# Kernel tuning notes

Measured on AMD Instinct MI355X. Metric: run time of the kernel, lower is better.

## Reference

```python
import jax, jax.numpy as jnp
import numpy as np

E = 16      # num experts
K = 2       # top-k
EPS = np.finfo(float).eps


def setup_inputs() -> dict:
    key = jax.random.key(0)
    k1, k2, k3 = jax.random.split(key, 3)
    B, D_IN, D_OUT = 16384, 1024, 512
    x = jax.random.normal(k1, (B, D_IN), dtype=jnp.float32)
    w_router = jax.random.normal(k2, (D_IN, E), dtype=jnp.float32) * 0.02
    w_experts = jax.random.normal(k3, (E, D_IN, D_OUT), dtype=jnp.float32) * 0.02
    return {"x": x, "w_router": w_router, "w_experts": w_experts}


def reference(x, w_router, w_experts):
    # --- noisy_top_k_gating (eval path: clean logits, no noise) ---
    logits = x @ w_router                      # [B, E]
    top_vals, top_idx = jax.lax.top_k(logits, K)   # [B, K]
    top_gates = jax.nn.softmax(top_vals, axis=1)   # softmax over top-k logits
    B = x.shape[0]
    gates = jnp.zeros_like(logits).at[jnp.arange(B)[:, None], top_idx].set(top_gates)  # [B, E]

    # --- per-expert encode (dense form; zero gates null out non-dispatched pairs,
    #     matching SparseDispatcher's sparse dispatch/combine math exactly) ---
    expert_out = jnp.einsum('bd,edh->beh', x, w_experts)  # [B, E, d_out]

    # --- SparseDispatcher.combine: exp -> gate-weight -> index_add -> eps clamp -> log ---
    combined = jnp.einsum('be,beh->bh', gates, jnp.exp(expert_out))  # [B, d_out]
    combined = jnp.where(combined == 0, jnp.asarray(EPS, combined.dtype), combined)
    return jnp.log(combined)
```

## Files before the change

kernel.cpp:

```cpp
#include <hip/hip_runtime.h>
#include <hip/hip_bf16.h>
#include <stdint.h>

typedef unsigned short u16_t;
typedef unsigned int   u32_t;

#define B_ROWS  16384
#define D_IN    1024
#define D_OUT   512
#define NEXP    16
#define CNT_STRIDE 16
#define EPSF    2.2204460492503131e-16f

using short8  = __attribute__((ext_vector_type(8))) short;
using floatx4 = __attribute__((ext_vector_type(4))) float;

__device__ __forceinline__ u16_t f2bf(float f) {
    u32_t u = __float_as_uint(f);
    u += 0x7fffu + ((u >> 16) & 1u);
    return (u16_t)(u >> 16);
}

__device__ __forceinline__ void gload_lds16(const void* g, void* l) {
    __builtin_amdgcn_global_load_lds(
        (const __attribute__((address_space(1))) void*)g,
        (__attribute__((address_space(3))) void*)l, 16, 0, 0);
}

__global__ __launch_bounds__(256) void prep_kernel(
        const float* __restrict__ wr, float* __restrict__ wrT,
        const float* __restrict__ we, u16_t* __restrict__ wT,
        int* __restrict__ counts) {
    int b = blockIdx.x, t = threadIdx.x;
    if (b < 64) {
        int i = b * 256 + t;
        int e = i >> 10, d = i & 1023;
        wrT[i] = wr[d * NEXP + e];
    } else if (b == 64) {
        counts[t] = 0;
    } else {
        int bb = b - 65;
        int e  = bb >> 8;
        int k0 = ((bb >> 1) & 127) * 8;
        int n  = (bb & 1) * 256 + t;
        const float* src = we + ((size_t)e * D_IN + k0) * D_OUT + n;
        union { u16_t us[8]; uint4 v; } p;
        #pragma unroll
        for (int j = 0; j < 8; ++j) p.us[j] = f2bf(src[(size_t)j * D_OUT]);
        *(uint4*)(wT + ((size_t)e * D_OUT + n) * D_IN + k0) = p.v;
    }
}

__global__ __launch_bounds__(256) void router_kernel(
        const float* __restrict__ x, const float* __restrict__ wrT,
        int* __restrict__ counts, int* __restrict__ rowlist,
        float* __restrict__ gatelist, u16_t* __restrict__ xb) {
    __shared__ int hist[NEXP], base[NEXP], hist2[NEXP];
    __shared__ unsigned char eidx_sh[16][2];
    __shared__ float g_sh[16][2];

    int t = threadIdx.x;
    if (t < NEXP) { hist[t] = 0; hist2[t] = 0; }
    __syncthreads();

    int lr = t >> 5, c = t & 31;
    int row0 = blockIdx.x * 16 + lr * 2;
    const float* xr = x + (size_t)row0 * D_IN + c * 4;
    const float4* wr4 = (const float4*)wrT;

    double acc[2][NEXP];
    #pragma unroll
    for (int rr = 0; rr < 2; ++rr)
        #pragma unroll
        for (int e = 0; e < NEXP; ++e) acc[rr][e] = 0.0;

    for (int i = 0; i < 8; ++i) {
        int d = c * 4 + i * 128;
        float4 xv[2];
        #pragma unroll
        for (int rr = 0; rr < 2; ++rr)
            xv[rr] = *(const float4*)(xr + (size_t)rr * D_IN + i * 128);
        if (xb) {
            #pragma unroll
            for (int rr = 0; rr < 2; ++rr) {
                uint2 pk;
                pk.x = (u32_t)f2bf(xv[rr].x) | ((u32_t)f2bf(xv[rr].y) << 16);
                pk.y = (u32_t)f2bf(xv[rr].z) | ((u32_t)f2bf(xv[rr].w) << 16);
                *(uint2*)(xb + (size_t)(row0 + rr) * D_IN + d) = pk;
            }
        }
        int f4 = c + i * 32;
        #pragma unroll
        for (int e = 0; e < NEXP; ++e) {
            float4 wv = wr4[e * 256 + f4];
            #pragma unroll
            for (int rr = 0; rr < 2; ++rr) {
                acc[rr][e] += (double)xv[rr].x * (double)wv.x;
                acc[rr][e] += (double)xv[rr].y * (double)wv.y;
                acc[rr][e] += (double)xv[rr].z * (double)wv.z;
                acc[rr][e] += (double)xv[rr].w * (double)wv.w;
            }
        }
    }
    #pragma unroll
    for (int rr = 0; rr < 2; ++rr)
        #pragma unroll
        for (int e = 0; e < NEXP; ++e) {
            acc[rr][e] += __shfl_xor(acc[rr][e], 1);
            acc[rr][e] += __shfl_xor(acc[rr][e], 2);
            acc[rr][e] += __shfl_xor(acc[rr][e], 4);
            acc[rr][e] += __shfl_xor(acc[rr][e], 8);
            acc[rr][e] += __shfl_xor(acc[rr][e], 16);
        }
    if (c == 0) {
        #pragma unroll
        for (int rr = 0; rr < 2; ++rr) {
            int i1 = 0; double v1 = acc[rr][0];
            #pragma unroll
            for (int e = 1; e < NEXP; ++e) if (acc[rr][e] > v1) { v1 = acc[rr][e]; i1 = e; }
            int i2 = -1; double v2 = -1.0e300;
            #pragma unroll
            for (int e = 0; e < NEXP; ++e) if (e != i1 && acc[rr][e] > v2) { v2 = acc[rr][e]; i2 = e; }
            double ed = exp(v2 - v1);
            double s = 1.0 + ed;
            int lrow = lr * 2 + rr;
            eidx_sh[lrow][0] = (unsigned char)i1; g_sh[lrow][0] = (float)(1.0 / s);
            eidx_sh[lrow][1] = (unsigned char)i2; g_sh[lrow][1] = (float)(ed / s);
            atomicAdd(&hist[i1], 1);
            atomicAdd(&hist[i2], 1);
        }
    }
    __syncthreads();
    if (t < NEXP) base[t] = atomicAdd(&counts[t * CNT_STRIDE], hist[t]);
    __syncthreads();
    if (t < 32) {
        int r = t >> 1, sl = t & 1;
        int e = eidx_sh[r][sl];
        int pos = base[e] + atomicAdd(&hist2[e], 1);
        rowlist[e * B_ROWS + pos] = ((blockIdx.x * 16 + r) << 1) | sl;
        gatelist[e * B_ROWS + pos] = g_sh[r][sl];
    }
}

template<bool USE_CONTRIB>
__global__ __launch_bounds__(256) void moe_gemm_bf16(
        const u16_t* __restrict__ xb, const u16_t* __restrict__ wT,
        const int* __restrict__ counts, const int* __restrict__ rowlist,
        const float* __restrict__ gatelist,
        float* __restrict__ out, float* __restrict__ contrib) {
    int bid = blockIdx.x;
    int s   = bid >> 3;
    int e   = ((bid & 7) << 1) | (s >> 9);
    s &= 511;
    int tx = s & 3, ty = s >> 2;
    int n_e = counts[e * CNT_STRIDE];
    if (ty * 128 >= n_e) return;
    int n0 = tx * 128;

    __shared__ u16_t Ash[128 * 64];
    __shared__ u16_t Bsh[128 * 64];
    __shared__ int   rid_sh[128];
    __shared__ float gt_sh[128];

    int t = threadIdx.x;
    if (t < 128) {
        int gi = ty * 128 + t;
        int v = 0; float g = 0.f;
        if (gi < n_e) { v = rowlist[e * B_ROWS + gi]; g = gatelist[e * B_ROWS + gi]; }
        rid_sh[t] = v; gt_sh[t] = g;
    }
    __syncthreads();

    int lane = t & 63, wv = t >> 6;

    const u16_t* asrc[4];
    const u16_t* bsrc[4];
    #pragma unroll
    for (int r = 0; r < 4; ++r) {
        int i   = r * 256 + wv * 64 + lane;
        int row = i >> 3;
        int ss  = (i & 7) ^ (row & 7);
        asrc[r] = xb + (size_t)(rid_sh[row] >> 1) * D_IN + ss * 8;
        bsrc[r] = wT + ((size_t)e * D_OUT + n0 + row) * D_IN + ss * 8;
    }

    int wm = wv >> 1, wn = wv & 1;
    int lm = lane & 15, q = lane >> 4;
    int l7 = lm & 7;

    floatx4 acc[4][4];
    #pragma unroll
    for (int mi = 0; mi < 4; ++mi)
        #pragma unroll
        for (int ni = 0; ni < 4; ++ni)
            acc[mi][ni] = (floatx4){0.f, 0.f, 0.f, 0.f};

    for (int it = 0; it < D_IN / 64; ++it) {
        if (it) __syncthreads();
        #pragma unroll
        for (int r = 0; r < 4; ++r) {
            gload_lds16(asrc[r], (char*)Ash + r * 4096 + wv * 1024);
            gload_lds16(bsrc[r], (char*)Bsh + r * 4096 + wv * 1024);
            asrc[r] += 64; bsrc[r] += 64;
        }
        __syncthreads();

        #pragma unroll
        for (int kk = 0; kk < 2; ++kk) {
            int sw = ((((kk << 2) | q) ^ l7) << 3);
            short8 afr[4], bfr[4];
            #pragma unroll
            for (int f = 0; f < 4; ++f) {
                afr[f] = *(const short8*)(Ash + ((wm * 64 + f * 16 + lm) << 6) + sw);
                bfr[f] = *(const short8*)(Bsh + ((wn * 64 + f * 16 + lm) << 6) + sw);
            }
            #pragma unroll
            for (int mi = 0; mi < 4; ++mi)
                #pragma unroll
                for (int ni = 0; ni < 4; ++ni)
                    acc[mi][ni] = __builtin_amdgcn_mfma_f32_16x16x32_bf16(
                        afr[mi], bfr[ni], acc[mi][ni], 0, 0, 0);
        }
    }

    #pragma unroll
    for (int mi = 0; mi < 4; ++mi) {
        int rbase = wm * 64 + mi * 16 + q * 4;
        #pragma unroll
        for (int r = 0; r < 4; ++r) {
            int row = rbase + r;
            int gi = ty * 128 + row;
            bool ok = gi < n_e;
            int v = rid_sh[row];
            float g = gt_sh[row];
            size_t orow = (size_t)(v >> 1) * D_OUT;
            #pragma unroll
            for (int ni = 0; ni < 4; ++ni) {
                int c = n0 + wn * 64 + ni * 16 + lm;
                float val = g * __expf(acc[mi][ni][r]);
                if (ok) {
                    if (USE_CONTRIB) {
                        float* dst = (v & 1) ? contrib : out;
                        dst[orow + c] = val;
                    } else {
                        atomicAdd(&out[orow + c], val);
                    }
                }
            }
        }
    }
}

template<bool USE_CONTRIB>
__global__ __launch_bounds__(256) void moe_gemm(
        const float* __restrict__ x, const float* __restrict__ w,
        const int* __restrict__ counts, const int* __restrict__ rowlist,
        const float* __restrict__ gatelist,
        float* __restrict__ out, float* __restrict__ contrib) {
    int e = blockIdx.z;
    int n_e = counts[e * CNT_STRIDE];
    int ty = blockIdx.y;
    if (ty * 128 >= n_e) return;
    int n0 = blockIdx.x * 128;

    __shared__ u16_t Ash[128][40];
    __shared__ u32_t Bsh[16][132];
    __shared__ int   rid_sh[128];
    __shared__ float gt_sh[128];

    int t = threadIdx.x;
    if (t < 128) {
        int gi = ty * 128 + t;
        int v = 0; float g = 0.f;
        if (gi < n_e) { v = rowlist[e * B_ROWS + gi]; g = gatelist[e * B_ROWS + gi]; }
        rid_sh[t] = v; gt_sh[t] = g;
    }
    __syncthreads();

    int ar = t >> 1, ah = t & 1;
    const float* xptr = x + (size_t)(rid_sh[ar] >> 1) * D_IN + ah * 16;
    int bkp = t >> 4, bng = t & 15;
    const float* wptr = w + (size_t)e * (D_IN * D_OUT)
                          + (size_t)(2 * bkp) * D_OUT + n0 + bng * 8;

    int lane = t & 63, wv = t >> 6;
    int wm = wv >> 1, wn = wv & 1;
    int lm = lane & 15, q = lane >> 4;

    floatx4 acc[4][4];
    #pragma unroll
    for (int mi = 0; mi < 4; ++mi)
        #pragma unroll
        for (int ni = 0; ni < 4; ++ni)
            acc[mi][ni] = (floatx4){0.f, 0.f, 0.f, 0.f};

    for (int it = 0; it < D_IN / 32; ++it) {
        float4 av0 = *(const float4*)(xptr + 0);
        float4 av1 = *(const float4*)(xptr + 4);
        float4 av2 = *(const float4*)(xptr + 8);
        float4 av3 = *(const float4*)(xptr + 12);
        xptr += 32;
        float4 b0 = *(const float4*)(wptr + 0);
        float4 b1 = *(const float4*)(wptr + 4);
        float4 b2 = *(const float4*)(wptr + D_OUT);
        float4 b3 = *(const float4*)(wptr + D_OUT + 4);
        wptr += 32 * D_OUT;

        __syncthreads();
        {
            union { u16_t us[16]; uint4 v[2]; } ap;
            float af[16] = {av0.x, av0.y, av0.z, av0.w, av1.x, av1.y, av1.z, av1.w,
                            av2.x, av2.y, av2.z, av2.w, av3.x, av3.y, av3.z, av3.w};
            #pragma unroll
            for (int j = 0; j < 16; ++j) ap.us[j] = f2bf(af[j]);
            *(uint4*)(&Ash[ar][ah * 16])     = ap.v[0];
            *(uint4*)(&Ash[ar][ah * 16 + 8]) = ap.v[1];
        }
        {
            union { u32_t up[8]; uint4 v[2]; } bp;
            bp.up[0] = (u32_t)f2bf(b0.x) | ((u32_t)f2bf(b2.x) << 16);
            bp.up[1] = (u32_t)f2bf(b0.y) | ((u32_t)f2bf(b2.y) << 16);
            bp.up[2] = (u32_t)f2bf(b0.z) | ((u32_t)f2bf(b2.z) << 16);
            bp.up[3] = (u32_t)f2bf(b0.w) | ((u32_t)f2bf(b2.w) << 16);
            bp.up[4] = (u32_t)f2bf(b1.x) | ((u32_t)f2bf(b3.x) << 16);
            bp.up[5] = (u32_t)f2bf(b1.y) | ((u32_t)f2bf(b3.y) << 16);
            bp.up[6] = (u32_t)f2bf(b1.z) | ((u32_t)f2bf(b3.z) << 16);
            bp.up[7] = (u32_t)f2bf(b1.w) | ((u32_t)f2bf(b3.w) << 16);
            *(uint4*)(&Bsh[bkp][bng * 8])     = bp.v[0];
            *(uint4*)(&Bsh[bkp][bng * 8 + 4]) = bp.v[1];
        }
        __syncthreads();

        short8 afr[4];
        #pragma unroll
        for (int mi = 0; mi < 4; ++mi)
            afr[mi] = *(const short8*)(&Ash[wm * 64 + mi * 16 + lm][q * 8]);
        short8 bfr[4];
        #pragma unroll
        for (int ni = 0; ni < 4; ++ni) {
            int nn = wn * 64 + ni * 16 + lm;
            union { uint4 u; short8 s; } cv;
            cv.u.x = Bsh[q * 4 + 0][nn];
            cv.u.y = Bsh[q * 4 + 1][nn];
            cv.u.z = Bsh[q * 4 + 2][nn];
            cv.u.w = Bsh[q * 4 + 3][nn];
            bfr[ni] = cv.s;
        }
        #pragma unroll
        for (int mi = 0; mi < 4; ++mi)
            #pragma unroll
            for (int ni = 0; ni < 4; ++ni)
                acc[mi][ni] = __builtin_amdgcn_mfma_f32_16x16x32_bf16(
                    afr[mi], bfr[ni], acc[mi][ni], 0, 0, 0);
    }

    #pragma unroll
    for (int mi = 0; mi < 4; ++mi) {
        int rbase = wm * 64 + mi * 16 + q * 4;
        #pragma unroll
        for (int r = 0; r < 4; ++r) {
            int row = rbase + r;
            int gi = ty * 128 + row;
            bool ok = gi < n_e;
            int v = rid_sh[row];
            float g = gt_sh[row];
            size_t orow = (size_t)(v >> 1) * D_OUT;
            #pragma unroll
            for (int ni = 0; ni < 4; ++ni) {
                int c = n0 + wn * 64 + ni * 16 + lm;
                float val = g * __expf(acc[mi][ni][r]);
                if (ok) {
                    if (USE_CONTRIB) {
                        float* dst = (v & 1) ? contrib : out;
                        dst[orow + c] = val;
                    } else {
                        atomicAdd(&out[orow + c], val);
                    }
                }
            }
        }
    }
}

__global__ __launch_bounds__(256) void combine_add_log(
        float* __restrict__ out, const float* __restrict__ contrib, int n4) {
    int i = blockIdx.x * blockDim.x + threadIdx.x;
    if (i >= n4) return;
    float4 a = ((const float4*)out)[i];
    float4 b = ((const float4*)contrib)[i];
    float4 r;
    float s;
    s = a.x + b.x; s = (s == 0.f) ? EPSF : s; r.x = __logf(s);
    s = a.y + b.y; s = (s == 0.f) ? EPSF : s; r.y = __logf(s);
    s = a.z + b.z; s = (s == 0.f) ? EPSF : s; r.z = __logf(s);
    s = a.w + b.w; s = (s == 0.f) ? EPSF : s; r.w = __logf(s);
    ((float4*)out)[i] = r;
}

__global__ __launch_bounds__(256) void log_inplace(float* __restrict__ out, int n4) {
    int i = blockIdx.x * blockDim.x + threadIdx.x;
    if (i >= n4) return;
    float4 a = ((float4*)out)[i];
    float4 r;
    float s;
    s = a.x; s = (s == 0.f) ? EPSF : s; r.x = __logf(s);
    s = a.y; s = (s == 0.f) ? EPSF : s; r.y = __logf(s);
    s = a.z; s = (s == 0.f) ? EPSF : s; r.z = __logf(s);
    s = a.w; s = (s == 0.f) ? EPSF : s; r.w = __logf(s);
    ((float4*)out)[i] = r;
}

extern "C" void kernel_launch(void* const* d_in, const int* in_sizes, int n_in,
                              void* d_out, int out_size, void* d_ws, size_t ws_size,
                              hipStream_t stream) {
    const float* x  = (const float*)d_in[0];
    const float* wr = (const float*)d_in[1];
    const float* we = (const float*)d_in[2];
    float* out = (float*)d_out;
    char* ws = (char*)d_ws;

    size_t off = 0;
    int*   counts  = (int*)(ws + off);   off += 1024;
    int*   rowlist = (int*)(ws + off);   off += (size_t)NEXP * B_ROWS * 4;
    float* gates   = (float*)(ws + off); off += (size_t)NEXP * B_ROWS * 4;
    float* wrT     = (float*)(ws + off); off += (size_t)NEXP * D_IN * 4;
    float* contrib = (float*)(ws + off); off += (size_t)B_ROWS * D_OUT * 4;
    size_t tier2_need = off;
    u16_t* xb      = (u16_t*)(ws + off); off += (size_t)B_ROWS * D_IN * 2;
    u16_t* wTb     = (u16_t*)(ws + off); off += (size_t)NEXP * D_IN * D_OUT * 2;
    size_t tier3_need = off;

    bool tier3 = ws_size >= tier3_need;
    bool tier2 = ws_size >= tier2_need;

    prep_kernel<<<tier3 ? (65 + NEXP * 256) : 65, 256, 0, stream>>>(
        wr, wrT, we, wTb, counts);
    router_kernel<<<B_ROWS / 16, 256, 0, stream>>>(
        x, wrT, counts, rowlist, gates, tier3 ? xb : (u16_t*)nullptr);

    int n4 = B_ROWS * D_OUT / 4;

    if (tier3) {
        moe_gemm_bf16<true><<<8192, 256, 0, stream>>>(
            xb, wTb, counts, rowlist, gates, out, contrib);
        combine_add_log<<<(n4 + 255) / 256, 256, 0, stream>>>(out, contrib, n4);
    } else if (tier2) {
        dim3 g(D_OUT / 128, B_ROWS / 128, NEXP);
        moe_gemm<true><<<g, 256, 0, stream>>>(x, we, counts, rowlist, gates, out, contrib);
        combine_add_log<<<(n4 + 255) / 256, 256, 0, stream>>>(out, contrib, n4);
    } else {
        dim3 g(D_OUT / 128, B_ROWS / 128, NEXP);
        hipMemsetAsync(out, 0, (size_t)B_ROWS * D_OUT * 4, stream);
        moe_gemm<false><<<g, 256, 0, stream>>>(x, we, counts, rowlist, gates, out, nullptr);
        log_inplace<<<(n4 + 255) / 256, 256, 0, stream>>>(out, n4);
    }
}
```

Baseline: 248.5 us.

## Use fp32 router accumulation and stage router weights in LDS

The router kernel now accumulates logits in fp32 instead of fp64 and stages the transposed router weights into shared memory in two 512-column phases via global_load_lds, rather than reading them from global memory per thread. x loads are batched four float4s at a time per phase. This removes slow fp64 FMAs and redundant global weight reads. The risk is that top-k selection changes on near-tied logits because fp32 accumulation is less accurate than fp64.

```diff
diff --git a/kernel.cpp b/kernel.cpp
--- a/kernel.cpp
+++ b/kernel.cpp
@@ -55,53 +55,77 @@
         const float* __restrict__ x, const float* __restrict__ wrT,
         int* __restrict__ counts, int* __restrict__ rowlist,
         float* __restrict__ gatelist, u16_t* __restrict__ xb) {
+    __shared__ float wsh[NEXP * 512];
     __shared__ int hist[NEXP], base[NEXP], hist2[NEXP];
     __shared__ unsigned char eidx_sh[16][2];
     __shared__ float g_sh[16][2];
 
     int t = threadIdx.x;
     if (t < NEXP) { hist[t] = 0; hist2[t] = 0; }
-    __syncthreads();
-
+
+    int lane = t & 63, wv = t >> 6;
     int lr = t >> 5, c = t & 31;
     int row0 = blockIdx.x * 16 + lr * 2;
-    const float* xr = x + (size_t)row0 * D_IN + c * 4;
-    const float4* wr4 = (const float4*)wrT;
-
-    double acc[2][NEXP];
+
+    float acc[2][NEXP];
     #pragma unroll
     for (int rr = 0; rr < 2; ++rr)
         #pragma unroll
-        for (int e = 0; e < NEXP; ++e) acc[rr][e] = 0.0;
-
-    for (int i = 0; i < 8; ++i) {
-        int d = c * 4 + i * 128;
-        float4 xv[2];
+        for (int e = 0; e < NEXP; ++e) acc[rr][e] = 0.f;
+
+    #pragma unroll
+    for (int ph = 0; ph < 2; ++ph) {
+        if (ph) __syncthreads();
+        #pragma unroll
+        for (int r = 0; r < 8; ++r) {
+            int s  = r * 256 + wv * 64 + lane;
+            int e  = s >> 7, d4 = s & 127;
+            gload_lds16(wrT + e * D_IN + ph * 512 + d4 * 4,
+                        (char*)wsh + r * 4096 + wv * 1024);
+        }
+        float4 xv[2][4];
         #pragma unroll
         for (int rr = 0; rr < 2; ++rr)
-            xv[rr] = *(const float4*)(xr + (size_t)rr * D_IN + i * 128);
+            #pragma unroll
+            for (int i = 0; i < 4; ++i)
+                xv[rr][i] = *(const float4*)(x + (size_t)(row0 + rr) * D_IN
+                                               + ph * 512 + c * 4 + i * 128);
+        #pragma unroll
+        for (int rr = 0; rr < 2; ++rr)
+            #pragma unroll
+            for (int i = 0; i < 4; ++i)
+                asm volatile("" : "+v"(xv[rr][i].x), "+v"(xv[rr][i].y),
+                                  "+v"(xv[rr][i].z), "+v"(xv[rr][i].w));
         if (xb) {
             #pragma unroll
-            for (int rr = 0; rr < 2; ++rr) {
-                uint2 pk;
-                pk.x = (u32_t)f2bf(xv[rr].x) | ((u32_t)f2bf(xv[rr].y) << 16);
-                pk.y = (u32_t)f2bf(xv[rr].z) | ((u32_t)f2bf(xv[rr].w) << 16);
-                *(uint2*)(xb + (size_t)(row0 + rr) * D_IN + d) = pk;
+            for (int rr = 0; rr < 2; ++rr)
+                #pragma unroll
+                for (int i = 0; i < 4; ++i) {
+                    uint2 pk;
+                    pk.x = (u32_t)f2bf(xv[rr][i].x) | ((u32_t)f2bf(xv[rr][i].y) << 16);
+                    pk.y = (u32_t)f2bf(xv[rr][i].z) | ((u32_t)f2bf(xv[rr][i].w) << 16);
+                    *(uint2*)(xb + (size_t)(row0 + rr) * D_IN
+                                 + ph * 512 + c * 4 + i * 128) = pk;
+                }
+        }
+        __syncthreads();
+        #pragma unroll
+        for (int i = 0; i < 4; ++i) {
+            int fo = c * 4 + i * 128;
+            #pragma unroll
+            for (int e = 0; e < NEXP; ++e) {
+                float4 wv4 = *(const float4*)(&wsh[e * 512 + fo]);
+                #pragma unroll
+                for (int rr = 0; rr < 2; ++rr) {
+                    acc[rr][e] += xv[rr][i].x * wv4.x;
+                    acc[rr][e] += xv[rr][i].y * wv4.y;
+                    acc[rr][e] += xv[rr][i].z * wv4.z;
+                    acc[rr][e] += xv[rr][i].w * wv4.w;
+                }
             }
         }
-        int f4 = c + i * 32;
-        #pragma unroll
-        for (int e = 0; e < NEXP; ++e) {
-            float4 wv = wr4[e * 256 + f4];
-            #pragma unroll
-            for (int rr = 0; rr < 2; ++rr) {
-                acc[rr][e] += (double)xv[rr].x * (double)wv.x;
-                acc[rr][e] += (double)xv[rr].y * (double)wv.y;
-                acc[rr][e] += (double)xv[rr].z * (double)wv.z;
-                acc[rr][e] += (double)xv[rr].w * (double)wv.w;
-            }
-        }
-    }
+    }
+
     #pragma unroll
     for (int rr = 0; rr < 2; ++rr)
         #pragma unroll
@@ -115,17 +139,17 @@
     if (c == 0) {
         #pragma unroll
         for (int rr = 0; rr < 2; ++rr) {
-            int i1 = 0; double v1 = acc[rr][0];
+            int i1 = 0; float v1 = acc[rr][0];
             #pragma unroll
             for (int e = 1; e < NEXP; ++e) if (acc[rr][e] > v1) { v1 = acc[rr][e]; i1 = e; }
-            int i2 = -1; double v2 = -1.0e300;
+            int i2 = -1; float v2 = -3.0e38f;
             #pragma unroll
             for (int e = 0; e < NEXP; ++e) if (e != i1 && acc[rr][e] > v2) { v2 = acc[rr][e]; i2 = e; }
-            double ed = exp(v2 - v1);
-            double s = 1.0 + ed;
+            float ed = expf(v2 - v1);
+            float s = 1.0f + ed;
             int lrow = lr * 2 + rr;
-            eidx_sh[lrow][0] = (unsigned char)i1; g_sh[lrow][0] = (float)(1.0 / s);
-            eidx_sh[lrow][1] = (unsigned char)i2; g_sh[lrow][1] = (float)(ed / s);
+            eidx_sh[lrow][0] = (unsigned char)i1; g_sh[lrow][0] = 1.0f / s;
+            eidx_sh[lrow][1] = (unsigned char)i2; g_sh[lrow][1] = ed / s;
             atomicAdd(&hist[i1], 1);
             atomicAdd(&hist[i2], 1);
         }
```

New measurement: 234.6 us. 1.06x faster.
